# Performance work log

Measured on AMD Instinct MI355X. Metric: run time of the kernel, lower is better.

## Reference

```python
import jax, jax.numpy as jnp
import numpy as np

B, N, D, E, K = 4, 4096, 2048, 128, 8


def setup_inputs() -> dict:
    key = jax.random.key(0)
    kx, kw, kb = jax.random.split(key, 3)
    x = jax.random.normal(kx, (B, N, D), dtype=jnp.float32)
    # nn.Linear(input_dim, num_experts): weight [E, D], bias [E]
    bound = 1.0 / np.sqrt(D)
    W = jax.random.uniform(kw, (E, D), dtype=jnp.float32, minval=-bound, maxval=bound)
    b = jax.random.uniform(kb, (E,), dtype=jnp.float32, minval=-bound, maxval=bound)
    return {"x": x, "W": W, "b": b}


def reference(x, W, b):
    # gate logits: [B, N, E]
    gate_logits = jnp.einsum("bnd,ed->bne", x, W) + b
    # top-k over experts
    topk_values, topk_indices = jax.lax.top_k(gate_logits, K)  # [B,N,K]
    topk_gates = jax.nn.softmax(topk_values, axis=-1)          # [B,N,K]
    # scatter normalized gates back into dense [B,N,E]
    onehot = jax.nn.one_hot(topk_indices, E, dtype=topk_gates.dtype)  # [B,N,K,E]
    full_gates = jnp.einsum("bnke,bnk->bne", onehot, topk_gates)
    return full_gates, topk_indices
```

## Files before the change

kernel.cpp:

```cpp
#include <hip/hip_runtime.h>
#include <cfloat>

#define TOKENS 16384
#define DDIM   2048
#define NEXP   128
#define KTOP   8
#define MB     64
#define CH     64
#define NCH    (DDIM / CH)
#define NTHR   512

typedef float    f32x4 __attribute__((ext_vector_type(4)));
typedef _Float16 f16x8 __attribute__((ext_vector_type(8)));

#define WFRAG_N (8 * NCH * 2 * 64)

__device__ __forceinline__ unsigned short f16bits(float f) {
    _Float16 h = (_Float16)f;
    return __builtin_bit_cast(unsigned short, h);
}
__device__ __forceinline__ float f16tof(unsigned short u) {
    return (float)__builtin_bit_cast(_Float16, u);
}

__global__ __launch_bounds__(256, 1) void wfrag_kernel(
    const float* __restrict__ W, uint4* __restrict__ wf)
{
    int id   = blockIdx.x * 256 + threadIdx.x;
    int lane = id & 63;
    int ks   = (id >> 6) & 1;
    int c    = (id >> 7) & (NCH - 1);
    int eb   = id >> 12;
    int e    = eb * 16 + (lane & 15);
    int k0   = c * CH + ks * 32 + (lane >> 4) * 8;
    const float* src = W + (size_t)e * DDIM + k0;
    unsigned hw[4], mw[4];
#pragma unroll
    for (int p = 0; p < 4; ++p) {
        float f0 = src[2 * p], f1 = src[2 * p + 1];
        unsigned short h0 = f16bits(f0), h1 = f16bits(f1);
        unsigned short m0 = f16bits((f0 - f16tof(h0)) * 4096.0f);
        unsigned short m1 = f16bits((f1 - f16tof(h1)) * 4096.0f);
        hw[p] = (unsigned)h0 | ((unsigned)h1 << 16);
        mw[p] = (unsigned)m0 | ((unsigned)m1 << 16);
    }
    wf[id]           = make_uint4(hw[0], hw[1], hw[2], hw[3]);
    wf[WFRAG_N + id] = make_uint4(mw[0], mw[1], mw[2], mw[3]);
}

__device__ __forceinline__ void insert8(float (&vals)[8], int (&idxs)[8], float v, int e) {
    bool c[8];
#pragma unroll
    for (int p = 0; p < 8; ++p) c[p] = v > vals[p];
#pragma unroll
    for (int p = 7; p >= 1; --p) {
        vals[p] = c[p] ? (c[p - 1] ? vals[p - 1] : v) : vals[p];
        idxs[p] = c[p] ? (c[p - 1] ? idxs[p - 1] : e) : idxs[p];
    }
    vals[0] = c[0] ? v : vals[0];
    idxs[0] = c[0] ? e : idxs[0];
}

__device__ __forceinline__ void chunk_barrier() {
    asm volatile("s_waitcnt lgkmcnt(0)" ::: "memory");
    __builtin_amdgcn_sched_barrier(0);
    __builtin_amdgcn_s_barrier();
    __builtin_amdgcn_sched_barrier(0);
}

__global__ __launch_bounds__(NTHR, 1) void router_kernel(
    const float* __restrict__ x, const uint4* __restrict__ wf,
    const float* __restrict__ b, float* __restrict__ out_gates,
    float* __restrict__ out_idx)
{
    __shared__ __align__(16) char smem[66560];
    float* lg  = (float*)smem;
    float* plv = (float*)(smem + 33792);
    int*   pli = (int*)(smem + 50176);

    const int tid  = threadIdx.x;
    const int lane = tid & 63;
    const int wid  = tid >> 6;
    const int tok0 = blockIdx.x * MB;

    const uint4* WFH = wf;
    const uint4* WFM = wf + WFRAG_N;

    f32x4 acc1[4], acc2[4];
#pragma unroll
    for (int mf = 0; mf < 4; ++mf) {
        acc1[mf] = (f32x4){0.f, 0.f, 0.f, 0.f};
        acc2[mf] = (f32x4){0.f, 0.f, 0.f, 0.f};
    }

    const float4* x4 = (const float4*)x;
    const int xr0 = tid >> 4, xr1 = 32 + (tid >> 4), xq = tid & 15;
    const size_t xoff0 = (size_t)(tok0 + xr0) * (DDIM / 4) + xq;
    const size_t xoff1 = (size_t)(tok0 + xr1) * (DDIM / 4) + xq;
    const int xb0 = xr0 * 128 + (((xq >> 1) ^ (xr0 & 7)) << 4) + (xq & 1) * 8;
    const int xb1 = xr1 * 128 + (((xq >> 1) ^ (xr1 & 7)) << 4) + (xq & 1) * 8;

    float4 sxA[2], sxB[2];
    uint4  wA[4], wB[4];

    auto loadW = [&](int c, uint4 (&wreg)[4]) {
#pragma unroll
        for (int ks = 0; ks < 2; ++ks) {
            int idx = ((wid * NCH + c) * 2 + ks) * 64 + lane;
            wreg[ks]     = WFH[idx];
            wreg[2 + ks] = WFM[idx];
        }
    };
    auto convertX = [&](const float4 (&sx)[2], char* ldsDst) {
#pragma unroll
        for (int r = 0; r < 2; ++r) {
            const float4 v = sx[r];
            unsigned short h0 = f16bits(v.x), h1 = f16bits(v.y);
            unsigned short h2 = f16bits(v.z), h3 = f16bits(v.w);
            unsigned short m0 = f16bits((v.x - f16tof(h0)) * 4096.0f);
            unsigned short m1 = f16bits((v.y - f16tof(h1)) * 4096.0f);
            unsigned short m2 = f16bits((v.z - f16tof(h2)) * 4096.0f);
            unsigned short m3 = f16bits((v.w - f16tof(h3)) * 4096.0f);
            uint2 hv = make_uint2((unsigned)h0 | ((unsigned)h1 << 16),
                                  (unsigned)h2 | ((unsigned)h3 << 16));
            uint2 mv = make_uint2((unsigned)m0 | ((unsigned)m1 << 16),
                                  (unsigned)m2 | ((unsigned)m3 << 16));
            const int byteoff = r ? xb1 : xb0;
            *(uint2*)(ldsDst + byteoff)         = hv;
            *(uint2*)(ldsDst + 16384 + byteoff) = mv;
        }
    };

    sxA[0] = x4[xoff0];  sxA[1] = x4[xoff1];
    loadW(0, wA);
    sxB[0] = x4[xoff0 + 16];  sxB[1] = x4[xoff1 + 16];
    convertX(sxA, smem);
    chunk_barrier();

    auto step = [&](int c, uint4 (&wCur)[4], uint4 (&wNext)[4],
                    float4 (&sxCur)[2], float4 (&sxNext)[2],
                    char* ldsCur, char* ldsNext) {
        if (c + 2 < NCH) {
            sxNext[0] = x4[xoff0 + (size_t)(c + 2) * 16];
            sxNext[1] = x4[xoff1 + (size_t)(c + 2) * 16];
        }
        if (c + 1 < NCH) loadW(c + 1, wNext);

#pragma unroll
        for (int ks = 0; ks < 2; ++ks) {
            f16x8 ah[4], am[4];
#pragma unroll
            for (int mf = 0; mf < 4; ++mf) {
                int row = 16 * mf + (lane & 15);
                int byteoff = row * 128 +
                    ((((ks << 2) | (lane >> 4)) ^ (row & 7)) << 4);
                ah[mf] = *(const f16x8*)(ldsCur + byteoff);
                am[mf] = *(const f16x8*)(ldsCur + 16384 + byteoff);
            }
            f16x8 wh = __builtin_bit_cast(f16x8, wCur[ks]);
            f16x8 wm = __builtin_bit_cast(f16x8, wCur[2 + ks]);
#pragma unroll
            for (int mf = 0; mf < 4; ++mf) {
                acc1[mf] = __builtin_amdgcn_mfma_f32_16x16x32_f16(
                    ah[mf], wh, acc1[mf], 0, 0, 0);
                acc2[mf] = __builtin_amdgcn_mfma_f32_16x16x32_f16(
                    ah[mf], wm, acc2[mf], 0, 0, 0);
                acc2[mf] = __builtin_amdgcn_mfma_f32_16x16x32_f16(
                    am[mf], wh, acc2[mf], 0, 0, 0);
            }
        }

        if (c + 1 < NCH) convertX(sxCur, ldsNext);
        chunk_barrier();
    };

    for (int cc = 0; cc < NCH; cc += 2) {
        step(cc,     wA, wB, sxB, sxA, smem,        smem + 8192);
        step(cc + 1, wB, wA, sxA, sxB, smem + 8192, smem);
    }

    const float bb = b[wid * 16 + (lane & 15)];
#pragma unroll
    for (int mf = 0; mf < 4; ++mf)
#pragma unroll
        for (int r = 0; r < 4; ++r) {
            int t = 16 * mf + (lane >> 4) * 4 + r;
            int e = wid * 16 + (lane & 15);
            lg[t * 132 + e] =
                fmaf(acc2[mf][r], 0.000244140625f, acc1[mf][r]) + bb;
        }
    __syncthreads();

    {
        int tt = tid >> 3, p = tid & 7;
        float vals[8]; int idxs[8];
#pragma unroll
        for (int k = 0; k < 8; ++k) { vals[k] = -FLT_MAX; idxs[k] = 0; }
        const float* row = &lg[tt * 132 + p * 16];
#pragma unroll
        for (int q = 0; q < 16; ++q)
            insert8(vals, idxs, row[q], p * 16 + q);
#pragma unroll
        for (int k = 0; k < 8; ++k) {
            plv[tid * 8 + k] = vals[k];
            pli[tid * 8 + k] = idxs[k];
        }
    }
    __syncthreads();

    float g[8]; int fidx[8];
    const bool active = (tid < MB);
    if (active) {
        float vals[8]; int idxs[8];
#pragma unroll
        for (int k = 0; k < 8; ++k) { vals[k] = -FLT_MAX; idxs[k] = 0; }
        for (int p = 0; p < 8; ++p) {
#pragma unroll
            for (int k = 0; k < 8; ++k)
                insert8(vals, idxs, plv[(tid * 8 + p) * 8 + k], pli[(tid * 8 + p) * 8 + k]);
        }
        float mx = vals[0];
        float s = 0.0f;
#pragma unroll
        for (int k = 0; k < 8; ++k) { g[k] = __expf(vals[k] - mx); s += g[k]; }
        float inv = 1.0f / s;
#pragma unroll
        for (int k = 0; k < 8; ++k) { g[k] *= inv; fidx[k] = idxs[k]; }
#pragma unroll
        for (int k = 0; k < 8; ++k)
            out_idx[(size_t)(tok0 + tid) * KTOP + k] = (float)idxs[k];
    }
    for (int f = tid; f < MB * 132; f += NTHR) lg[f] = 0.0f;
    __syncthreads();

    if (active) {
#pragma unroll
        for (int k = 0; k < 8; ++k) lg[tid * 132 + fidx[k]] = g[k];
    }
    __syncthreads();

    for (int f = tid; f < MB * (NEXP / 4); f += NTHR) {
        int m = f >> 5, e4 = f & 31;
        float4 v = *(const float4*)&lg[m * 132 + e4 * 4];
        ((float4*)out_gates)[(size_t)(tok0 + m) * (NEXP / 4) + e4] = v;
    }
}

extern "C" void kernel_launch(void* const* d_in, const int* in_sizes, int n_in,
                              void* d_out, int out_size, void* d_ws, size_t ws_size,
                              hipStream_t stream) {
    const float* x = (const float*)d_in[0];
    const float* W = (const float*)d_in[1];
    const float* b = (const float*)d_in[2];

    float* out_gates = (float*)d_out;
    float* out_idx   = out_gates + (size_t)TOKENS * NEXP;

    uint4* wf = (uint4*)d_ws;

    wfrag_kernel<<<dim3(WFRAG_N / 256), dim3(256), 0, stream>>>(W, wf);
    router_kernel<<<dim3(TOKENS / MB), dim3(NTHR), 0, stream>>>(x, wf, b, out_gates, out_idx);
}
```

Baseline: 63.00 us.

## Deepen x prefetch to four chunks and split top-k over four partials

The x loads now run four chunks ahead using four rotating register sets instead of two, so more global-load latency is hidden behind the MFMA work on each chunk. The first top-k stage now uses 256 threads scanning 32 experts each instead of 512 scanning 16. Partial results are stored with a stride of 9 to avoid LDS bank conflicts, which halves the per-token merge in the final stage and shrinks shared memory. The cost is more live registers for the extra prefetch buffers, and a longer serial scan in the first top-k stage.

Result: faster. 53.86 us (-14.5%).

```diff
diff --git a/kernel.cpp b/kernel.cpp
--- a/kernel.cpp
+++ b/kernel.cpp
@@ -73,10 +73,10 @@
     const float* __restrict__ b, float* __restrict__ out_gates,
     float* __restrict__ out_idx)
 {
-    __shared__ __align__(16) char smem[66560];
+    __shared__ __align__(16) char smem[52224];
     float* lg  = (float*)smem;
     float* plv = (float*)(smem + 33792);
-    int*   pli = (int*)(smem + 50176);
+    int*   pli = (int*)(smem + 43008);
 
     const int tid  = threadIdx.x;
     const int lane = tid & 63;
@@ -100,9 +100,13 @@
     const int xb0 = xr0 * 128 + (((xq >> 1) ^ (xr0 & 7)) << 4) + (xq & 1) * 8;
     const int xb1 = xr1 * 128 + (((xq >> 1) ^ (xr1 & 7)) << 4) + (xq & 1) * 8;
 
-    float4 sxA[2], sxB[2];
+    float4 S0[2], S1[2], S2[2], S3[2];
     uint4  wA[4], wB[4];
 
+    auto loadX = [&](int c, float4 (&S)[2]) {
+        S[0] = x4[xoff0 + (size_t)c * 16];
+        S[1] = x4[xoff1 + (size_t)c * 16];
+    };
     auto loadW = [&](int c, uint4 (&wreg)[4]) {
 #pragma unroll
         for (int ks = 0; ks < 2; ++ks) {
@@ -131,19 +135,10 @@
         }
     };
 
-    sxA[0] = x4[xoff0];  sxA[1] = x4[xoff1];
-    loadW(0, wA);
-    sxB[0] = x4[xoff0 + 16];  sxB[1] = x4[xoff1 + 16];
-    convertX(sxA, smem);
-    chunk_barrier();
-
-    auto step = [&](int c, uint4 (&wCur)[4], uint4 (&wNext)[4],
-                    float4 (&sxCur)[2], float4 (&sxNext)[2],
-                    char* ldsCur, char* ldsNext) {
-        if (c + 2 < NCH) {
-            sxNext[0] = x4[xoff0 + (size_t)(c + 2) * 16];
-            sxNext[1] = x4[xoff1 + (size_t)(c + 2) * 16];
-        }
+    auto step = [&](int c, float4 (&Sload)[2], float4 (&Scvt)[2],
+                    uint4 (&wCur)[4], uint4 (&wNext)[4],
+                    char* bufCur, char* bufNext) {
+        if (c + 4 < NCH) loadX(c + 4, Sload);
         if (c + 1 < NCH) loadW(c + 1, wNext);
 
 #pragma unroll
@@ -154,8 +149,8 @@
                 int row = 16 * mf + (lane & 15);
                 int byteoff = row * 128 +
                     ((((ks << 2) | (lane >> 4)) ^ (row & 7)) << 4);
-                ah[mf] = *(const f16x8*)(ldsCur + byteoff);
-                am[mf] = *(const f16x8*)(ldsCur + 16384 + byteoff);
+                ah[mf] = *(const f16x8*)(bufCur + byteoff);
+                am[mf] = *(const f16x8*)(bufCur + 16384 + byteoff);
             }
             f16x8 wh = __builtin_bit_cast(f16x8, wCur[ks]);
             f16x8 wm = __builtin_bit_cast(f16x8, wCur[2 + ks]);
@@ -170,13 +165,25 @@
             }
         }
 
-        if (c + 1 < NCH) convertX(sxCur, ldsNext);
+        if (c + 1 < NCH) convertX(Scvt, bufNext);
         chunk_barrier();
     };
 
-    for (int cc = 0; cc < NCH; cc += 2) {
-        step(cc,     wA, wB, sxB, sxA, smem,        smem + 8192);
-        step(cc + 1, wB, wA, sxA, sxB, smem + 8192, smem);
+    loadX(0, S0);
+    loadX(1, S1);
+    loadW(0, wA);
+    loadX(2, S2);
+    loadX(3, S3);
+    convertX(S0, smem);
+    chunk_barrier();
+
+    char* buf0 = smem;
+    char* buf1 = smem + 8192;
+    for (int cc = 0; cc < NCH; cc += 4) {
+        step(cc,     S0, S1, wA, wB, buf0, buf1);
+        step(cc + 1, S1, S2, wB, wA, buf1, buf0);
+        step(cc + 2, S2, S3, wA, wB, buf0, buf1);
+        step(cc + 3, S3, S0, wB, wA, buf1, buf0);
     }
 
     const float bb = b[wid * 16 + (lane & 15)];
@@ -191,19 +198,18 @@
         }
     __syncthreads();
 
-    {
-        int tt = tid >> 3, p = tid & 7;
+    if (tid < 256) {
+        int tt = tid >> 2, p = tid & 3;
         float vals[8]; int idxs[8];
 #pragma unroll
         for (int k = 0; k < 8; ++k) { vals[k] = -FLT_MAX; idxs[k] = 0; }
-        const float* row = &lg[tt * 132 + p * 16];
-#pragma unroll
-        for (int q = 0; q < 16; ++q)
-            insert8(vals, idxs, row[q], p * 16 + q);
+        const float* row = &lg[tt * 132 + p * 32];
+        for (int q = 0; q < 32; ++q)
+            insert8(vals, idxs, row[q], p * 32 + q);
 #pragma unroll
         for (int k = 0; k < 8; ++k) {
-            plv[tid * 8 + k] = vals[k];
-            pli[tid * 8 + k] = idxs[k];
+            plv[tid * 9 + k] = vals[k];
+            pli[tid * 9 + k] = idxs[k];
         }
     }
     __syncthreads();
@@ -214,10 +220,10 @@
         float vals[8]; int idxs[8];
 #pragma unroll
         for (int k = 0; k < 8; ++k) { vals[k] = -FLT_MAX; idxs[k] = 0; }
-        for (int p = 0; p < 8; ++p) {
+        for (int p = 0; p < 4; ++p) {
 #pragma unroll
             for (int k = 0; k < 8; ++k)
-                insert8(vals, idxs, plv[(tid * 8 + p) * 8 + k], pli[(tid * 8 + p) * 8 + k]);
+                insert8(vals, idxs, plv[(tid * 4 + p) * 9 + k], pli[(tid * 4 + p) * 9 + k]);
         }
         float mx = vals[0];
         float s = 0.0f;
```
